# Performance work log

Hardware: AMD Instinct MI355X
Metric: run time of the kernel (lower is better)

## Reference

```python
import jax, jax.numpy as jnp
import numpy as np

B, SQ, SC, D = 16, 1024, 1024, 768
H = 2 * D  # 1536, fc width
NCLS = 2


def setup_inputs() -> dict:
    key = jax.random.key(0)
    ks = jax.random.split(key, 8)
    q = jax.random.normal(ks[0], (B, SQ, D), jnp.float32)
    c = jax.random.normal(ks[1], (B, SC, D), jnp.float32)
    mask_q = jax.random.randint(ks[2], (B, SQ), 0, 2).astype(jnp.int32)
    mask_c = jax.random.randint(ks[3], (B, SC), 0, 2).astype(jnp.int32)
    labels = jax.random.randint(ks[4], (B,), 0, NCLS)
    # torch nn.Linear convention: weight [out, in], y = x @ W.T + b
    W1 = jax.random.normal(ks[5], (H, H), jnp.float32) * 0.02
    b1 = jnp.zeros((H,), jnp.float32)
    W2 = jax.random.normal(ks[6], (NCLS, H), jnp.float32) * 0.02
    b2 = jnp.zeros((NCLS,), jnp.float32)
    return dict(q=q, c=c, mask_q=mask_q, mask_c=mask_c, labels=labels,
                W1=W1, b1=b1, W2=W2, b2=b2)


def reference(q, c, mask_q, mask_c, labels, W1, b1, W2, b2):
    # masked QK^T score matrix: [B, SQ, SC]
    s = jnp.einsum('bik,bjk->bij', q, c)
    s = s * mask_q[:, :, None].astype(s.dtype) * mask_c[:, None, :].astype(s.dtype)
    s = jnp.where(s == 0.0, -jnp.inf, s)  # x[x == 0.0] = -inf
    p = jnp.nan_to_num(jax.nn.softmax(s, axis=2))   # softmax over context axis
    pp = jnp.nan_to_num(jax.nn.softmax(s, axis=1))  # softmax over question axis
    a = jnp.einsum('bjk,bij->bk', c, p)   # weighted combine into context feats
    bb = jnp.einsum('bik,bij->bk', q, pp)  # weighted combine into question feats
    x = jnp.concatenate([a, bb], axis=1)  # [B, 1536]
    x = jnp.tanh(x @ W1.T + b1)           # fc1 + tanh (dropout = identity in eval)
    logits = x @ W2.T + b2                # fc2
    logp = jax.nn.log_softmax(logits, axis=1)  # LogSoftmax(dim=1)
    # NLLLoss (mean reduction)
    loss = -jnp.mean(jnp.take_along_axis(logp, labels[:, None], axis=1))
    return (loss, logp)
```

## Files before the change

### kernel.cpp

```cpp
#include <hip/hip_runtime.h>
#include <math.h>

#define B_   16
#define SQ_  1024
#define SC_  1024
#define D_   768
#define H_   1536
#define BK   32
#define LDK  40

typedef __attribute__((ext_vector_type(4))) float f32x4;
typedef __attribute__((ext_vector_type(8))) short bf16x8;

__device__ __forceinline__ unsigned cvtpk(float x, float y) {
  unsigned r;
  asm("v_cvt_pk_bf16_f32 %0, %1, %2" : "=v"(r) : "v"(x), "v"(y));
  return r;
}

__device__ __forceinline__ void split4(float4 v, uint2& hi, uint2& lo) {
  unsigned h01 = cvtpk(v.x, v.y);
  unsigned h23 = cvtpk(v.z, v.w);
  float h0 = __uint_as_float(h01 << 16);
  float h1 = __uint_as_float(h01 & 0xFFFF0000u);
  float h2 = __uint_as_float(h23 << 16);
  float h3 = __uint_as_float(h23 & 0xFFFF0000u);
  hi = make_uint2(h01, h23);
  lo = make_uint2(cvtpk(v.x - h0, v.y - h1), cvtpk(v.z - h2, v.w - h3));
}

__global__ __launch_bounds__(256) void compact_kernel(
    const int* __restrict__ mask_q, const int* __restrict__ mask_c,
    int* __restrict__ idx_q, int* __restrict__ idx_c, int* __restrict__ cnt)
{
  int which = blockIdx.x & 1;
  int b     = blockIdx.x >> 1;
  const int* m = (which ? mask_c : mask_q) + b * 1024;
  int* idx     = (which ? idx_c : idx_q) + b * 1024;

  __shared__ int tsum[256];
  int t = threadIdx.x;
  int v[4], s = 0;
#pragma unroll
  for (int e = 0; e < 4; ++e) { v[e] = (m[t * 4 + e] != 0) ? 1 : 0; s += v[e]; }
  tsum[t] = s;
  __syncthreads();
  for (int off = 1; off < 256; off <<= 1) {
    int add = (t >= off) ? tsum[t - off] : 0;
    __syncthreads();
    tsum[t] += add;
    __syncthreads();
  }
  int pos = tsum[t] - s;
#pragma unroll
  for (int e = 0; e < 4; ++e) {
    if (v[e]) idx[pos++] = t * 4 + e;
  }
  if (t == 255) cnt[b * 2 + which] = tsum[255];
}

__global__ __launch_bounds__(256) void gemm_mfma_kernel(
    const float* __restrict__ q, const float* __restrict__ c,
    const int* __restrict__ idx_q, const int* __restrict__ idx_c,
    const int* __restrict__ cnt, float* __restrict__ S)
{
  __shared__ unsigned short Ah[2][64][LDK];
  __shared__ unsigned short Al[2][64][LDK];
  __shared__ unsigned short Bh[2][64][LDK];
  __shared__ unsigned short Bl[2][64][LDK];

  const int b  = blockIdx.z;
  const int i0 = blockIdx.y * 64;
  const int j0 = blockIdx.x * 64;
  const int nq = cnt[2 * b], nc = cnt[2 * b + 1];
  if (i0 >= nq || j0 >= nc) return;

  const int t    = threadIdx.x;
  const int lane = t & 63;
  const int w    = t >> 6;

  const int srow = t >> 2;
  const int kc   = (t & 3) * 4;
  const int fr   = lane & 15;
  const int fq   = lane >> 4;
  const int kg   = fq * 8;

  const int rq = idx_q[b * 1024 + min(i0 + srow, nq - 1)];
  const int rc = idx_c[b * 1024 + min(j0 + srow, nc - 1)];
  const float* qrowP = q + ((size_t)b * SQ_ + rq) * D_;
  const float* crowP = c + ((size_t)b * SC_ + rc) * D_;

  f32x4 acc[4] = {};

  float4 av0 = *(const float4*)(qrowP + kc);
  float4 av1 = *(const float4*)(qrowP + kc + 16);
  float4 bv0 = *(const float4*)(crowP + kc);
  float4 bv1 = *(const float4*)(crowP + kc + 16);
  {
    uint2 hi, lo;
    split4(av0, hi, lo); *(uint2*)&Ah[0][srow][kc]      = hi; *(uint2*)&Al[0][srow][kc]      = lo;
    split4(av1, hi, lo); *(uint2*)&Ah[0][srow][kc + 16] = hi; *(uint2*)&Al[0][srow][kc + 16] = lo;
    split4(bv0, hi, lo); *(uint2*)&Bh[0][srow][kc]      = hi; *(uint2*)&Bl[0][srow][kc]      = lo;
    split4(bv1, hi, lo); *(uint2*)&Bh[0][srow][kc + 16] = hi; *(uint2*)&Bl[0][srow][kc + 16] = lo;
  }
  __syncthreads();

  int cur = 0;
  for (int k0 = 0; k0 < D_; k0 += BK) {
    const int next = k0 + BK;
    const bool has_next = (next < D_);
    if (has_next) {
      av0 = *(const float4*)(qrowP + next + kc);
      av1 = *(const float4*)(qrowP + next + kc + 16);
      bv0 = *(const float4*)(crowP + next + kc);
      bv1 = *(const float4*)(crowP + next + kc + 16);
    }

    bf16x8 b_h = *reinterpret_cast<const bf16x8*>(&Bh[cur][w * 16 + fr][kg]);
    bf16x8 b_l = *reinterpret_cast<const bf16x8*>(&Bl[cur][w * 16 + fr][kg]);
#pragma unroll
    for (int m = 0; m < 4; ++m) {
      bf16x8 a_h = *reinterpret_cast<const bf16x8*>(&Ah[cur][m * 16 + fr][kg]);
      bf16x8 a_l = *reinterpret_cast<const bf16x8*>(&Al[cur][m * 16 + fr][kg]);
      acc[m] = __builtin_amdgcn_mfma_f32_16x16x32_bf16(a_h, b_h, acc[m], 0, 0, 0);
      acc[m] = __builtin_amdgcn_mfma_f32_16x16x32_bf16(a_h, b_l, acc[m], 0, 0, 0);
      acc[m] = __builtin_amdgcn_mfma_f32_16x16x32_bf16(a_l, b_h, acc[m], 0, 0, 0);
    }

    if (has_next) {
      int nxt = cur ^ 1;
      uint2 hi, lo;
      split4(av0, hi, lo); *(uint2*)&Ah[nxt][srow][kc]      = hi; *(uint2*)&Al[nxt][srow][kc]      = lo;
      split4(av1, hi, lo); *(uint2*)&Ah[nxt][srow][kc + 16] = hi; *(uint2*)&Al[nxt][srow][kc + 16] = lo;
      split4(bv0, hi, lo); *(uint2*)&Bh[nxt][srow][kc]      = hi; *(uint2*)&Bl[nxt][srow][kc]      = lo;
      split4(bv1, hi, lo); *(uint2*)&Bh[nxt][srow][kc + 16] = hi; *(uint2*)&Bl[nxt][srow][kc + 16] = lo;
    }
    __syncthreads();
    cur ^= 1;
  }

  const int col = j0 + w * 16 + fr;
  const bool cok = (col < nc);
#pragma unroll
  for (int m = 0; m < 4; ++m) {
    int rbase = i0 + m * 16 + fq * 4;
    float* Sp = S + ((size_t)b * SQ_ + rbase) * SC_ + col;
#pragma unroll
    for (int rr = 0; rr < 4; ++rr) {
      float v = acc[m][rr];
      bool valid = ((rbase + rr) < nq) && cok && (v != 0.f);
      Sp[(size_t)rr * SC_] = valid ? v : -INFINITY;
    }
  }
}

__global__ __launch_bounds__(256) void row_stats_kernel(
    const float* __restrict__ S, const int* __restrict__ cnt,
    float* __restrict__ rmE, float* __restrict__ riE)
{
  int w    = threadIdx.x >> 6;
  int lane = threadIdx.x & 63;
  int row  = blockIdx.x * 4 + w;
  int b = row >> 10, i = row & 1023;
  int nq_pad = (cnt[2 * b] + 63) & ~63;
  if (i >= nq_pad) return;
  int nc_pad = (cnt[2 * b + 1] + 63) & ~63;
  const float4* Sr = (const float4*)(S + (size_t)row * SC_);

  float m = -INFINITY, s = 0.f;
  int n4 = nc_pad >> 2;
  for (int j4 = lane; j4 < n4; j4 += 64) {
    float4 v = Sr[j4];
    float vm = fmaxf(fmaxf(v.x, v.y), fmaxf(v.z, v.w));
    if (vm > m) { s *= __expf(m - vm); m = vm; }
    if (m > -INFINITY) {
      s += __expf(v.x - m) + __expf(v.y - m) + __expf(v.z - m) + __expf(v.w - m);
    }
  }
#pragma unroll
  for (int o = 32; o; o >>= 1) {
    float om = __shfl_xor(m, o);
    float os = __shfl_xor(s, o);
    float nm = fmaxf(m, om);
    float e1 = (m == nm) ? 1.f : __expf(m - nm);
    float e2 = (om == nm) ? 1.f : __expf(om - nm);
    s = s * e1 + os * e2;
    m = nm;
  }
  if (lane == 0) {
    bool dead = !(s > 0.f);
    rmE[row] = dead ? INFINITY : m;
    riE[row] = dead ? 0.f : 1.0f / s;
  }
}

__global__ __launch_bounds__(1024) void col_pass_kernel(
    const float* __restrict__ S, const int* __restrict__ cnt,
    const float* __restrict__ rmE, const float* __restrict__ riE,
    float* __restrict__ cmE, float* __restrict__ ciE,
    float* __restrict__ colsum_p)
{
  __shared__ float redm[1024], reds[1024], redp[1024];

  int b  = blockIdx.y;
  int j0 = blockIdx.x * 64;
  int nq_pad = (cnt[2 * b] + 63) & ~63;
  int nc_pad = (cnt[2 * b + 1] + 63) & ~63;
  if (j0 >= nc_pad) return;
  int t  = threadIdx.x;

  int j     = j0 + (t & 63);
  int wv    = t >> 6;
  int chunk = nq_pad >> 4;
  int i0    = wv * chunk;
  const float* Sb  = S + ((size_t)b * SQ_ + i0) * SC_ + j;
  const float* rmb = rmE + b * SQ_ + i0;
  const float* rib = riE + b * SQ_ + i0;

  float cm = -INFINITY, cs = 0.f, cp = 0.f;
  for (int ii = 0; ii < chunk; ++ii) {
    float v = Sb[(size_t)ii * SC_];
    cp += __expf(v - rmb[ii]) * rib[ii];
    if (v > cm) { cs = cs * __expf(cm - v) + 1.0f; cm = v; }
    else if (cm > -INFINITY) cs += __expf(v - cm);
  }

  redm[t] = cm; reds[t] = cs; redp[t] = cp;
  __syncthreads();
  if (t < 64) {
    float m = redm[t], s = reds[t], p = redp[t];
#pragma unroll
    for (int wv2 = 1; wv2 < 16; ++wv2) {
      float om = redm[wv2 * 64 + t], os = reds[wv2 * 64 + t];
      float nm = fmaxf(m, om);
      float e1 = (m == nm) ? 1.f : __expf(m - nm);
      float e2 = (om == nm) ? 1.f : __expf(om - nm);
      s = s * e1 + os * e2; m = nm;
      p += redp[wv2 * 64 + t];
    }
    bool dead = !(s > 0.f);
    cmE[b * SC_ + j0 + t] = dead ? INFINITY : m;
    ciE[b * SC_ + j0 + t] = dead ? 0.f : 1.0f / s;
    colsum_p[b * SC_ + j0 + t] = p;
  }
}

__global__ __launch_bounds__(256) void rowsum_pp_kernel(
    const float* __restrict__ S, const int* __restrict__ cnt,
    const float* __restrict__ cmE, const float* __restrict__ ciE,
    float* __restrict__ rowsum_pp)
{
  int t = threadIdx.x;
  int row0 = blockIdx.x * 4;
  int b = row0 >> 10;
  int nq = cnt[2 * b];
  if ((row0 & 1023) >= nq) return;
  int nc_pad = (cnt[2 * b + 1] + 63) & ~63;

  int w = t >> 6, lane = t & 63;
  int row = row0 + w;
  const float4* Sr  = (const float4*)(S + (size_t)row * SC_);
  const float4* cm4 = (const float4*)(cmE + b * SC_);
  const float4* ci4 = (const float4*)(ciE + b * SC_);

  float accv = 0.f;
  int n4 = nc_pad >> 2;
  for (int j4 = lane; j4 < n4; j4 += 64) {
    float4 v = Sr[j4];
    float4 cm = cm4[j4];
    float4 ci = ci4[j4];
    accv += __expf(v.x - cm.x) * ci.x;
    accv += __expf(v.y - cm.y) * ci.y;
    accv += __expf(v.z - cm.z) * ci.z;
    accv += __expf(v.w - cm.w) * ci.w;
  }
#pragma unroll
  for (int o = 32; o; o >>= 1) accv += __shfl_xor(accv, o);
  if (lane == 0) rowsum_pp[row] = accv;
}

__global__ __launch_bounds__(256) void combine_kernel(
    const float* __restrict__ q, const float* __restrict__ c,
    const int* __restrict__ idx_q, const int* __restrict__ idx_c,
    const int* __restrict__ cnt,
    const float* __restrict__ colsum_p, const float* __restrict__ rowsum_pp,
    float* __restrict__ Xp)
{
  int jc = blockIdx.x;
  int op = blockIdx.y;
  int b  = blockIdx.z;
  int t  = threadIdx.x;

  int n = op ? cnt[2 * b] : cnt[2 * b + 1];
  const float* src = op ? (q + (size_t)b * SQ_ * D_) : (c + (size_t)b * SC_ * D_);
  const float* wv  = op ? (rowsum_pp + b * SQ_) : (colsum_p + b * SC_);
  const int*   idx = (op ? idx_q : idx_c) + b * 1024;

  float a0 = 0.f, a1 = 0.f, a2 = 0.f;
  int je = min(jc * 32 + 32, n);
  for (int j = jc * 32; j < je; ++j) {
    float wj = wv[j];
    const float* r = src + (size_t)idx[j] * D_;
    a0 += wj * r[t];
    a1 += wj * r[t + 256];
    a2 += wj * r[t + 512];
  }
  float* xp = Xp + ((size_t)jc * B_ + b) * H_ + op * D_;
  xp[t] = a0; xp[t + 256] = a1; xp[t + 512] = a2;
}

__global__ __launch_bounds__(256) void reduce_x_kernel(
    const float* __restrict__ Xp, float* __restrict__ X)
{
  int idx = blockIdx.x * 256 + threadIdx.x;
  float s = 0.f;
#pragma unroll
  for (int ch = 0; ch < 32; ++ch) s += Xp[(size_t)ch * B_ * H_ + idx];
  X[idx] = s;
}

__global__ __launch_bounds__(256) void fc1_kernel(
    const float* __restrict__ X, const float* __restrict__ W1,
    const float* __restrict__ b1, float* __restrict__ Y)
{
  int w = threadIdx.x >> 6, lane = threadIdx.x & 63;
  int h = blockIdx.x * 4 + w;
  const float4* wr = (const float4*)(W1 + (size_t)h * H_);
  float4 wv[6];
#pragma unroll
  for (int it = 0; it < 6; ++it) wv[it] = wr[it * 64 + lane];
  float bias = b1[h];

  for (int b = 0; b < B_; ++b) {
    const float4* x = (const float4*)(X + (size_t)b * H_);
    float accv = 0.f;
#pragma unroll
    for (int it = 0; it < 6; ++it) {
      float4 xv = x[it * 64 + lane];
      accv += xv.x * wv[it].x + xv.y * wv[it].y + xv.z * wv[it].z + xv.w * wv[it].w;
    }
#pragma unroll
    for (int o = 32; o; o >>= 1) accv += __shfl_xor(accv, o);
    if (lane == 0) Y[(size_t)b * H_ + h] = tanhf(accv + bias);
  }
}

__global__ __launch_bounds__(64) void fc2_loss_kernel(
    const float* __restrict__ Y, const float* __restrict__ W2,
    const float* __restrict__ b2, const int* __restrict__ labels,
    float* __restrict__ out)
{
  __shared__ float logp_s[B_][2];
  int t = threadIdx.x;
  if (t < 2 * B_) {
    int b = t >> 1, n = t & 1;
    const float* y = Y + (size_t)b * H_;
    const float* w = W2 + (size_t)n * H_;
    float accv = b2[n];
    for (int k = 0; k < H_; ++k) accv += y[k] * w[k];
    logp_s[b][n] = accv;
  }
  __syncthreads();
  if (t < B_) {
    float l0 = logp_s[t][0], l1 = logp_s[t][1];
    float m = fmaxf(l0, l1);
    float lse = m + logf(expf(l0 - m) + expf(l1 - m));
    logp_s[t][0] = l0 - lse;
    logp_s[t][1] = l1 - lse;
  }
  __syncthreads();
  if (t < 2 * B_) out[1 + t] = logp_s[t >> 1][t & 1];
  if (t == 0) {
    float loss = 0.f;
    for (int b = 0; b < B_; ++b) loss -= logp_s[b][labels[b]];
    out[0] = loss / (float)B_;
  }
}

extern "C" void kernel_launch(void* const* d_in, const int* in_sizes, int n_in,
                              void* d_out, int out_size, void* d_ws, size_t ws_size,
                              hipStream_t stream) {
  const float* q      = (const float*)d_in[0];
  const float* c      = (const float*)d_in[1];
  const int*   mask_q = (const int*)d_in[2];
  const int*   mask_c = (const int*)d_in[3];
  const int*   labels = (const int*)d_in[4];
  const float* W1     = (const float*)d_in[5];
  const float* b1     = (const float*)d_in[6];
  const float* W2     = (const float*)d_in[7];
  const float* b2     = (const float*)d_in[8];
  float* out = (float*)d_out;

  float* ws        = (float*)d_ws;
  float* S         = ws;
  float* rmE       = ws + (size_t)B_ * SQ_ * SC_;
  float* riE       = rmE + B_ * SQ_;
  float* cmE       = riE + B_ * SQ_;
  float* ciE       = cmE + B_ * SC_;
  float* colsum_p  = ciE + B_ * SC_;
  float* rowsum_pp = colsum_p + B_ * SC_;
  int*   cnt       = (int*)(rowsum_pp + B_ * SQ_);
  int*   idx_q     = cnt + 2 * B_;
  int*   idx_c     = idx_q + B_ * SQ_;
  float* Xp        = ws;
  float* X         = ws + 32 * B_ * H_;
  float* Y         = X + B_ * H_;

  compact_kernel<<<2 * B_, 256, 0, stream>>>(mask_q, mask_c, idx_q, idx_c, cnt);

  dim3 g1(SC_ / 64, SQ_ / 64, B_);
  gemm_mfma_kernel<<<g1, 256, 0, stream>>>(q, c, idx_q, idx_c, cnt, S);

  row_stats_kernel<<<(B_ * SQ_) / 4, 256, 0, stream>>>(S, cnt, rmE, riE);
  col_pass_kernel<<<dim3(SC_ / 64, B_), 1024, 0, stream>>>(S, cnt, rmE, riE,
                                                           cmE, ciE, colsum_p);
  rowsum_pp_kernel<<<(B_ * SQ_) / 4, 256, 0, stream>>>(S, cnt, cmE, ciE, rowsum_pp);

  combine_kernel<<<dim3(32, 2, B_), 256, 0, stream>>>(q, c, idx_q, idx_c, cnt,
                                                      colsum_p, rowsum_pp, Xp);
  reduce_x_kernel<<<(B_ * H_) / 256, 256, 0, stream>>>(Xp, X);
  fc1_kernel<<<H_ / 4, 256, 0, stream>>>(X, W1, b1, Y);
  fc2_loss_kernel<<<1, 64, 0, stream>>>(Y, W2, b2, labels, out);
}
```

Before: 158.4 us.

## Fuse softmax denominators into GEMM epilogue with persistent tile scheduler

The GEMM epilogue now computes unshifted exponentials in double precision, using a custom exp that avoids overflow, and atomically accumulates the row and column softmax denominators. This removes the separate row-stats pass and the max-tracking column pass. A persistent atomic tile queue over only the valid compacted tiles replaces the sparse 3D grid. A single pass2 kernel then produces both weighted sums, and the combine kernel writes X with atomics instead of a partial buffer plus a reduce kernel. The trade-offs are heavy double-precision atomics, per-row float atomics in pass2, and reliance on the scores staying within double exponent range.

```diff
diff --git a/kernel.cpp b/kernel.cpp
--- a/kernel.cpp
+++ b/kernel.cpp
@@ -29,6 +29,15 @@
   lo = make_uint2(cvtpk(v.x - h0, v.y - h1), cvtpk(v.z - h2, v.w - h3));
 }
 
+__device__ __forceinline__ double exp_pos(float s) {
+  float t = s * 1.4426950408889634f;
+  float n = floorf(t);
+  float p = exp2f(t - n);
+  long long e = (long long)n;
+  double scale = __longlong_as_double((unsigned long long)(e + 1023LL) << 52);
+  return (double)p * scale;
+}
+
 __global__ __launch_bounds__(256) void compact_kernel(
     const int* __restrict__ mask_q, const int* __restrict__ mask_c,
     int* __restrict__ idx_q, int* __restrict__ idx_c, int* __restrict__ cnt)
@@ -59,232 +68,207 @@
   if (t == 255) cnt[b * 2 + which] = tsum[255];
 }
 
+__global__ void tile_setup_kernel(const int* __restrict__ cnt, int* __restrict__ tmeta)
+{
+  if (threadIdx.x == 0) {
+    int off = 0;
+    for (int b = 0; b < B_; ++b) {
+      int ntq = (cnt[2 * b] + 63) >> 6;
+      int ntc = (cnt[2 * b + 1] + 63) >> 6;
+      tmeta[1 + b]  = off;
+      tmeta[17 + b] = ntc;
+      off += ntq * ntc;
+    }
+    tmeta[0]  = off;
+    tmeta[33] = 0;
+  }
+}
+
 __global__ __launch_bounds__(256) void gemm_mfma_kernel(
     const float* __restrict__ q, const float* __restrict__ c,
     const int* __restrict__ idx_q, const int* __restrict__ idx_c,
-    const int* __restrict__ cnt, float* __restrict__ S)
+    const int* __restrict__ cnt, int* __restrict__ tmeta,
+    float* __restrict__ S, double* __restrict__ R, double* __restrict__ C)
 {
   __shared__ unsigned short Ah[2][64][LDK];
   __shared__ unsigned short Al[2][64][LDK];
   __shared__ unsigned short Bh[2][64][LDK];
   __shared__ unsigned short Bl[2][64][LDK];
-
-  const int b  = blockIdx.z;
-  const int i0 = blockIdx.y * 64;
-  const int j0 = blockIdx.x * 64;
-  const int nq = cnt[2 * b], nc = cnt[2 * b + 1];
-  if (i0 >= nq || j0 >= nc) return;
+  __shared__ int tidx_s;
 
   const int t    = threadIdx.x;
   const int lane = t & 63;
   const int w    = t >> 6;
-
   const int srow = t >> 2;
   const int kc   = (t & 3) * 4;
   const int fr   = lane & 15;
   const int fq   = lane >> 4;
   const int kg   = fq * 8;
 
-  const int rq = idx_q[b * 1024 + min(i0 + srow, nq - 1)];
-  const int rc = idx_c[b * 1024 + min(j0 + srow, nc - 1)];
-  const float* qrowP = q + ((size_t)b * SQ_ + rq) * D_;
-  const float* crowP = c + ((size_t)b * SC_ + rc) * D_;
-
-  f32x4 acc[4] = {};
-
-  float4 av0 = *(const float4*)(qrowP + kc);
-  float4 av1 = *(const float4*)(qrowP + kc + 16);
-  float4 bv0 = *(const float4*)(crowP + kc);
-  float4 bv1 = *(const float4*)(crowP + kc + 16);
-  {
-    uint2 hi, lo;
-    split4(av0, hi, lo); *(uint2*)&Ah[0][srow][kc]      = hi; *(uint2*)&Al[0][srow][kc]      = lo;
-    split4(av1, hi, lo); *(uint2*)&Ah[0][srow][kc + 16] = hi; *(uint2*)&Al[0][srow][kc + 16] = lo;
-    split4(bv0, hi, lo); *(uint2*)&Bh[0][srow][kc]      = hi; *(uint2*)&Bl[0][srow][kc]      = lo;
-    split4(bv1, hi, lo); *(uint2*)&Bh[0][srow][kc + 16] = hi; *(uint2*)&Bl[0][srow][kc + 16] = lo;
-  }
-  __syncthreads();
-
-  int cur = 0;
-  for (int k0 = 0; k0 < D_; k0 += BK) {
-    const int next = k0 + BK;
-    const bool has_next = (next < D_);
-    if (has_next) {
-      av0 = *(const float4*)(qrowP + next + kc);
-      av1 = *(const float4*)(qrowP + next + kc + 16);
-      bv0 = *(const float4*)(crowP + next + kc);
-      bv1 = *(const float4*)(crowP + next + kc + 16);
-    }
-
-    bf16x8 b_h = *reinterpret_cast<const bf16x8*>(&Bh[cur][w * 16 + fr][kg]);
-    bf16x8 b_l = *reinterpret_cast<const bf16x8*>(&Bl[cur][w * 16 + fr][kg]);
+  const int total = tmeta[0];
+
+  while (true) {
+    if (t == 0) tidx_s = atomicAdd(&tmeta[33], 1);
+    __syncthreads();
+    const int idx = tidx_s;
+    if (idx >= total) break;
+
+    int bb = 0;
+#pragma unroll
+    for (int k = 1; k < 16; ++k) bb += (idx >= tmeta[1 + k]) ? 1 : 0;
+    const int rem = idx - tmeta[1 + bb];
+    const int ntc = tmeta[17 + bb];
+    const int ty  = rem / ntc;
+    const int tx  = rem - ty * ntc;
+    const int i0  = ty * 64, j0 = tx * 64;
+    const int nq  = cnt[2 * bb], nc = cnt[2 * bb + 1];
+
+    const int rq = idx_q[bb * 1024 + min(i0 + srow, nq - 1)];
+    const int rc = idx_c[bb * 1024 + min(j0 + srow, nc - 1)];
+    const float* qrowP = q + ((size_t)bb * SQ_ + rq) * D_;
+    const float* crowP = c + ((size_t)bb * SC_ + rc) * D_;
+
+    f32x4 acc[4] = {};
+
+    float4 av0 = *(const float4*)(qrowP + kc);
+    float4 av1 = *(const float4*)(qrowP + kc + 16);
+    float4 bv0 = *(const float4*)(crowP + kc);
+    float4 bv1 = *(const float4*)(crowP + kc + 16);
+    {
+      uint2 hi, lo;
+      split4(av0, hi, lo); *(uint2*)&Ah[0][srow][kc]      = hi; *(uint2*)&Al[0][srow][kc]      = lo;
+      split4(av1, hi, lo); *(uint2*)&Ah[0][srow][kc + 16] = hi; *(uint2*)&Al[0][srow][kc + 16] = lo;
+      split4(bv0, hi, lo); *(uint2*)&Bh[0][srow][kc]      = hi; *(uint2*)&Bl[0][srow][kc]      = lo;
+      split4(bv1, hi, lo); *(uint2*)&Bh[0][srow][kc + 16] = hi; *(uint2*)&Bl[0][srow][kc + 16] = lo;
+    }
+    __syncthreads();
+
+    int cur = 0;
+    for (int k0 = 0; k0 < D_; k0 += BK) {
+      const int next = k0 + BK;
+      const bool has_next = (next < D_);
+      if (has_next) {
+        av0 = *(const float4*)(qrowP + next + kc);
+        av1 = *(const float4*)(qrowP + next + kc + 16);
+        bv0 = *(const float4*)(crowP + next + kc);
+        bv1 = *(const float4*)(crowP + next + kc + 16);
+      }
+
+      bf16x8 b_h = *reinterpret_cast<const bf16x8*>(&Bh[cur][w * 16 + fr][kg]);
+      bf16x8 b_l = *reinterpret_cast<const bf16x8*>(&Bl[cur][w * 16 + fr][kg]);
+#pragma unroll
+      for (int m = 0; m < 4; ++m) {
+        bf16x8 a_h = *reinterpret_cast<const bf16x8*>(&Ah[cur][m * 16 + fr][kg]);
+        bf16x8 a_l = *reinterpret_cast<const bf16x8*>(&Al[cur][m * 16 + fr][kg]);
+        acc[m] = __builtin_amdgcn_mfma_f32_16x16x32_bf16(a_h, b_h, acc[m], 0, 0, 0);
+        acc[m] = __builtin_amdgcn_mfma_f32_16x16x32_bf16(a_h, b_l, acc[m], 0, 0, 0);
+        acc[m] = __builtin_amdgcn_mfma_f32_16x16x32_bf16(a_l, b_h, acc[m], 0, 0, 0);
+      }
+
+      if (has_next) {
+        int nxt = cur ^ 1;
+        uint2 hi, lo;
+        split4(av0, hi, lo); *(uint2*)&Ah[nxt][srow][kc]      = hi; *(uint2*)&Al[nxt][srow][kc]      = lo;
+        split4(av1, hi, lo); *(uint2*)&Ah[nxt][srow][kc + 16] = hi; *(uint2*)&Al[nxt][srow][kc + 16] = lo;
+        split4(bv0, hi, lo); *(uint2*)&Bh[nxt][srow][kc]      = hi; *(uint2*)&Bl[nxt][srow][kc]      = lo;
+        split4(bv1, hi, lo); *(uint2*)&Bh[nxt][srow][kc + 16] = hi; *(uint2*)&Bl[nxt][srow][kc + 16] = lo;
+      }
+      __syncthreads();
+      cur ^= 1;
+    }
+
+    double* rowAcc = reinterpret_cast<double*>(&Ah[0][0][0]);
+    const int col = j0 + w * 16 + fr;
+    const bool cok = (col < nc);
+    double colSum = 0.0;
 #pragma unroll
     for (int m = 0; m < 4; ++m) {
-      bf16x8 a_h = *reinterpret_cast<const bf16x8*>(&Ah[cur][m * 16 + fr][kg]);
-      bf16x8 a_l = *reinterpret_cast<const bf16x8*>(&Al[cur][m * 16 + fr][kg]);
-      acc[m] = __builtin_amdgcn_mfma_f32_16x16x32_bf16(a_h, b_h, acc[m], 0, 0, 0);
-      acc[m] = __builtin_amdgcn_mfma_f32_16x16x32_bf16(a_h, b_l, acc[m], 0, 0, 0);
-      acc[m] = __builtin_amdgcn_mfma_f32_16x16x32_bf16(a_l, b_h, acc[m], 0, 0, 0);
-    }
-
-    if (has_next) {
-      int nxt = cur ^ 1;
-      uint2 hi, lo;
-      split4(av0, hi, lo); *(uint2*)&Ah[nxt][srow][kc]      = hi; *(uint2*)&Al[nxt][srow][kc]      = lo;
-      split4(av1, hi, lo); *(uint2*)&Ah[nxt][srow][kc + 16] = hi; *(uint2*)&Al[nxt][srow][kc + 16] = lo;
-      split4(bv0, hi, lo); *(uint2*)&Bh[nxt][srow][kc]      = hi; *(uint2*)&Bl[nxt][srow][kc]      = lo;
-      split4(bv1, hi, lo); *(uint2*)&Bh[nxt][srow][kc + 16] = hi; *(uint2*)&Bl[nxt][srow][kc + 16] = lo;
-    }
-    __syncthreads();
-    cur ^= 1;
-  }
-
-  const int col = j0 + w * 16 + fr;
-  const bool cok = (col < nc);
-#pragma unroll
-  for (int m = 0; m < 4; ++m) {
-    int rbase = i0 + m * 16 + fq * 4;
-    float* Sp = S + ((size_t)b * SQ_ + rbase) * SC_ + col;
-#pragma unroll
-    for (int rr = 0; rr < 4; ++rr) {
-      float v = acc[m][rr];
-      bool valid = ((rbase + rr) < nq) && cok && (v != 0.f);
-      Sp[(size_t)rr * SC_] = valid ? v : -INFINITY;
-    }
-  }
-}
-
-__global__ __launch_bounds__(256) void row_stats_kernel(
+      int rbase = i0 + m * 16 + fq * 4;
+      float* Sp = S + ((size_t)bb * SQ_ + rbase) * SC_ + col;
+#pragma unroll
+      for (int rr = 0; rr < 4; ++rr) {
+        float v = acc[m][rr];
+        bool valid = ((rbase + rr) < nq) && cok && (v != 0.f);
+        Sp[(size_t)rr * SC_] = valid ? v : -INFINITY;
+        double e = valid ? exp_pos(v) : 0.0;
+        colSum += e;
+        double rsum = e;
+        rsum += __shfl_xor(rsum, 1);
+        rsum += __shfl_xor(rsum, 2);
+        rsum += __shfl_xor(rsum, 4);
+        rsum += __shfl_xor(rsum, 8);
+        if (fr == 0) rowAcc[w * 64 + m * 16 + fq * 4 + rr] = rsum;
+      }
+    }
+    colSum += __shfl_xor(colSum, 16);
+    colSum += __shfl_xor(colSum, 32);
+    if (fq == 0 && cok) atomicAdd(&C[bb * SC_ + col], colSum);
+    __syncthreads();
+    if (t < 64) {
+      double rs = rowAcc[t] + rowAcc[64 + t] + rowAcc[128 + t] + rowAcc[192 + t];
+      if ((i0 + t) < nq && rs != 0.0) atomicAdd(&R[bb * SQ_ + i0 + t], rs);
+    }
+    __syncthreads();
+  }
+}
+
+__global__ __launch_bounds__(1024) void pass2_kernel(
     const float* __restrict__ S, const int* __restrict__ cnt,
-    float* __restrict__ rmE, float* __restrict__ riE)
-{
-  int w    = threadIdx.x >> 6;
-  int lane = threadIdx.x & 63;
-  int row  = blockIdx.x * 4 + w;
-  int b = row >> 10, i = row & 1023;
-  int nq_pad = (cnt[2 * b] + 63) & ~63;
-  if (i >= nq_pad) return;
-  int nc_pad = (cnt[2 * b + 1] + 63) & ~63;
-  const float4* Sr = (const float4*)(S + (size_t)row * SC_);
-
-  float m = -INFINITY, s = 0.f;
-  int n4 = nc_pad >> 2;
-  for (int j4 = lane; j4 < n4; j4 += 64) {
-    float4 v = Sr[j4];
-    float vm = fmaxf(fmaxf(v.x, v.y), fmaxf(v.z, v.w));
-    if (vm > m) { s *= __expf(m - vm); m = vm; }
-    if (m > -INFINITY) {
-      s += __expf(v.x - m) + __expf(v.y - m) + __expf(v.z - m) + __expf(v.w - m);
-    }
-  }
-#pragma unroll
-  for (int o = 32; o; o >>= 1) {
-    float om = __shfl_xor(m, o);
-    float os = __shfl_xor(s, o);
-    float nm = fmaxf(m, om);
-    float e1 = (m == nm) ? 1.f : __expf(m - nm);
-    float e2 = (om == nm) ? 1.f : __expf(om - nm);
-    s = s * e1 + os * e2;
-    m = nm;
-  }
-  if (lane == 0) {
-    bool dead = !(s > 0.f);
-    rmE[row] = dead ? INFINITY : m;
-    riE[row] = dead ? 0.f : 1.0f / s;
-  }
-}
-
-__global__ __launch_bounds__(1024) void col_pass_kernel(
-    const float* __restrict__ S, const int* __restrict__ cnt,
-    const float* __restrict__ rmE, const float* __restrict__ riE,
-    float* __restrict__ cmE, float* __restrict__ ciE,
-    float* __restrict__ colsum_p)
-{
-  __shared__ float redm[1024], reds[1024], redp[1024];
+    const double* __restrict__ R, const double* __restrict__ C,
+    float* __restrict__ cp, float* __restrict__ rpp)
+{
+  __shared__ float lnR_lds[SQ_];
+  __shared__ float red[16][64];
 
   int b  = blockIdx.y;
   int j0 = blockIdx.x * 64;
   int nq_pad = (cnt[2 * b] + 63) & ~63;
   int nc_pad = (cnt[2 * b + 1] + 63) & ~63;
   if (j0 >= nc_pad) return;
-  int t  = threadIdx.x;
-
-  int j     = j0 + (t & 63);
-  int wv    = t >> 6;
+  int t = threadIdx.x;
+
+  if (t < nq_pad) {
+    double Ri = R[b * SQ_ + t];
+    lnR_lds[t] = (Ri > 0.0) ? (float)log(Ri) : INFINITY;
+  }
+  __syncthreads();
+
+  int lane = t & 63, wv = t >> 6;
+  int j = j0 + lane;
+  double Cj = C[b * SC_ + j];
+  float lnCj = (Cj > 0.0) ? (float)log(Cj) : INFINITY;
+
   int chunk = nq_pad >> 4;
-  int i0    = wv * chunk;
-  const float* Sb  = S + ((size_t)b * SQ_ + i0) * SC_ + j;
-  const float* rmb = rmE + b * SQ_ + i0;
-  const float* rib = riE + b * SQ_ + i0;
-
-  float cm = -INFINITY, cs = 0.f, cp = 0.f;
+  int i0 = wv * chunk;
+  const float* Sb = S + ((size_t)b * SQ_ + i0) * SC_ + j;
+
+  float cpAcc = 0.f;
   for (int ii = 0; ii < chunk; ++ii) {
+    int i = i0 + ii;
     float v = Sb[(size_t)ii * SC_];
-    cp += __expf(v - rmb[ii]) * rib[ii];
-    if (v > cm) { cs = cs * __expf(cm - v) + 1.0f; cm = v; }
-    else if (cm > -INFINITY) cs += __expf(v - cm);
-  }
-
-  redm[t] = cm; reds[t] = cs; redp[t] = cp;
+    cpAcc += __expf(v - lnR_lds[i]);
+    float e2 = __expf(v - lnCj);
+#pragma unroll
+    for (int o = 32; o; o >>= 1) e2 += __shfl_xor(e2, o);
+    if (lane == 0) atomicAdd(&rpp[b * SQ_ + i], e2);
+  }
+
+  red[wv][lane] = cpAcc;
   __syncthreads();
   if (t < 64) {
-    float m = redm[t], s = reds[t], p = redp[t];
-#pragma unroll
-    for (int wv2 = 1; wv2 < 16; ++wv2) {
-      float om = redm[wv2 * 64 + t], os = reds[wv2 * 64 + t];
-      float nm = fmaxf(m, om);
-      float e1 = (m == nm) ? 1.f : __expf(m - nm);
-      float e2 = (om == nm) ? 1.f : __expf(om - nm);
-      s = s * e1 + os * e2; m = nm;
-      p += redp[wv2 * 64 + t];
-    }
-    bool dead = !(s > 0.f);
-    cmE[b * SC_ + j0 + t] = dead ? INFINITY : m;
-    ciE[b * SC_ + j0 + t] = dead ? 0.f : 1.0f / s;
-    colsum_p[b * SC_ + j0 + t] = p;
-  }
-}
-
-__global__ __launch_bounds__(256) void rowsum_pp_kernel(
-    const float* __restrict__ S, const int* __restrict__ cnt,
-    const float* __restrict__ cmE, const float* __restrict__ ciE,
-    float* __restrict__ rowsum_pp)
-{
-  int t = threadIdx.x;
-  int row0 = blockIdx.x * 4;
-  int b = row0 >> 10;
-  int nq = cnt[2 * b];
-  if ((row0 & 1023) >= nq) return;
-  int nc_pad = (cnt[2 * b + 1] + 63) & ~63;
-
-  int w = t >> 6, lane = t & 63;
-  int row = row0 + w;
-  const float4* Sr  = (const float4*)(S + (size_t)row * SC_);
-  const float4* cm4 = (const float4*)(cmE + b * SC_);
-  const float4* ci4 = (const float4*)(ciE + b * SC_);
-
-  float accv = 0.f;
-  int n4 = nc_pad >> 2;
-  for (int j4 = lane; j4 < n4; j4 += 64) {
-    float4 v = Sr[j4];
-    float4 cm = cm4[j4];
-    float4 ci = ci4[j4];
-    accv += __expf(v.x - cm.x) * ci.x;
-    accv += __expf(v.y - cm.y) * ci.y;
-    accv += __expf(v.z - cm.z) * ci.z;
-    accv += __expf(v.w - cm.w) * ci.w;
-  }
-#pragma unroll
-  for (int o = 32; o; o >>= 1) accv += __shfl_xor(accv, o);
-  if (lane == 0) rowsum_pp[row] = accv;
+    float s = 0.f;
+#pragma unroll
+    for (int k = 0; k < 16; ++k) s += red[k][t];
+    cp[b * SC_ + j0 + t] = s;
+  }
 }
 
 __global__ __launch_bounds__(256) void combine_kernel(
     const float* __restrict__ q, const float* __restrict__ c,
     const int* __restrict__ idx_q, const int* __restrict__ idx_c,
     const int* __restrict__ cnt,
-    const float* __restrict__ colsum_p, const float* __restrict__ rowsum_pp,
-    float* __restrict__ Xp)
+    const float* __restrict__ cp, const float* __restrict__ rpp,
+    float* __restrict__ X)
 {
   int jc = blockIdx.x;
   int op = blockIdx.y;
@@ -293,7 +277,7 @@
 
   int n = op ? cnt[2 * b] : cnt[2 * b + 1];
   const float* src = op ? (q + (size_t)b * SQ_ * D_) : (c + (size_t)b * SC_ * D_);
-  const float* wv  = op ? (rowsum_pp + b * SQ_) : (colsum_p + b * SC_);
+  const float* wv  = op ? (rpp + b * SQ_) : (cp + b * SC_);
   const int*   idx = (op ? idx_q : idx_c) + b * 1024;
 
   float a0 = 0.f, a1 = 0.f, a2 = 0.f;
@@ -305,18 +289,10 @@
     a1 += wj * r[t + 256];
     a2 += wj * r[t + 512];
   }
-  float* xp = Xp + ((size_t)jc * B_ + b) * H_ + op * D_;
-  xp[t] = a0; xp[t + 256] = a1; xp[t + 512] = a2;
-}
-
-__global__ __launch_bounds__(256) void reduce_x_kernel(
-    const float* __restrict__ Xp, float* __restrict__ X)
-{
-  int idx = blockIdx.x * 256 + threadIdx.x;
-  float s = 0.f;
-#pragma unroll
-  for (int ch = 0; ch < 32; ++ch) s += Xp[(size_t)ch * B_ * H_ + idx];
-  X[idx] = s;
+  float* xp = X + (size_t)b * H_ + op * D_;
+  atomicAdd(&xp[t], a0);
+  atomicAdd(&xp[t + 256], a1);
+  atomicAdd(&xp[t + 512], a2);
 }
 
 __global__ __launch_bounds__(256) void fc1_kernel(
@@ -391,34 +367,32 @@
   const float* b2     = (const float*)d_in[8];
   float* out = (float*)d_out;
 
-  float* ws        = (float*)d_ws;
-  float* S         = ws;
-  float* rmE       = ws + (size_t)B_ * SQ_ * SC_;
-  float* riE       = rmE + B_ * SQ_;
-  float* cmE       = riE + B_ * SQ_;
-  float* ciE       = cmE + B_ * SC_;
-  float* colsum_p  = ciE + B_ * SC_;
-  float* rowsum_pp = colsum_p + B_ * SC_;
-  int*   cnt       = (int*)(rowsum_pp + B_ * SQ_);
-  int*   idx_q     = cnt + 2 * B_;
-  int*   idx_c     = idx_q + B_ * SQ_;
-  float* Xp        = ws;
-  float* X         = ws + 32 * B_ * H_;
-  float* Y         = X + B_ * H_;
+  float*  ws   = (float*)d_ws;
+  float*  S    = ws;
+  double* R    = (double*)(ws + (size_t)B_ * SQ_ * SC_);
+  double* C    = R + B_ * SQ_;
+  float*  cp   = (float*)(C + B_ * SC_);
+  float*  rpp  = cp + B_ * SC_;
+  int*    cnt  = (int*)(rpp + B_ * SQ_);
+  int*    tmeta = cnt + 2 * B_;
+  int*    idx_q = tmeta + 34;
+  int*    idx_c = idx_q + B_ * SQ_;
+  float*  X    = ws;
+  float*  Y    = ws + B_ * H_;
+
+  (void)hipMemsetAsync((void*)R, 0, (size_t)(2 * B_ * SQ_) * sizeof(double)
+                              + (size_t)(2 * B_ * SC_) * sizeof(float), stream);
 
   compact_kernel<<<2 * B_, 256, 0, stream>>>(mask_q, mask_c, idx_q, idx_c, cnt);
-
-  dim3 g1(SC_ / 64, SQ_ / 64, B_);
-  gemm_mfma_kernel<<<g1, 256, 0, stream>>>(q, c, idx_q, idx_c, cnt, S);
-
-  row_stats_kernel<<<(B_ * SQ_) / 4, 256, 0, stream>>>(S, cnt, rmE, riE);
-  col_pass_kernel<<<dim3(SC_ / 64, B_), 1024, 0, stream>>>(S, cnt, rmE, riE,
-                                                           cmE, ciE, colsum_p);
-  rowsum_pp_kernel<<<(B_ * SQ_) / 4, 256, 0, stream>>>(S, cnt, cmE, ciE, rowsum_pp);
-
+  tile_setup_kernel<<<1, 64, 0, stream>>>(cnt, tmeta);
+
+  gemm_mfma_kernel<<<1024, 256, 0, stream>>>(q, c, idx_q, idx_c, cnt, tmeta, S, R, C);
+
+  pass2_kernel<<<dim3(SC_ / 64, B_), 1024, 0, stream>>>(S, cnt, R, C, cp, rpp);
+
+  (void)hipMemsetAsync((void*)X, 0, (size_t)B_ * H_ * sizeof(float), stream);
   combine_kernel<<<dim3(32, 2, B_), 256, 0, stream>>>(q, c, idx_q, idx_c, cnt,
-                                                      colsum_p, rowsum_pp, Xp);
-  reduce_x_kernel<<<(B_ * H_) / 256, 256, 0, stream>>>(Xp, X);
+                                                      cp, rpp, X);
   fc1_kernel<<<H_ / 4, 256, 0, stream>>>(X, W1, b1, Y);
   fc2_loss_kernel<<<1, 64, 0, stream>>>(Y, W2, b2, labels, out);
 }
```

Result: slower. 164.0 us (+3.5%).

## Swizzle merged hi/lo GEMM LDS tiles and fold X reduction into atomics

Applied to the files above, without the earlier changes.

The GEMM now keeps the hi and lo bf16 halves of each row in a single 64-wide LDS row with an XOR swizzle, instead of four padded arrays. This is meant to cut LDS bank conflicts and the padding overhead on the MFMA operand reads. Separately, combine_kernel now atomically adds its partial sums straight into X, which compact_kernel zeroes first, so the Xp partial buffer and the reduce_x kernel launch are gone. The trade is atomic contention on X and a summation order that is no longer deterministic.

```diff
diff --git a/kernel.cpp b/kernel.cpp
--- a/kernel.cpp
+++ b/kernel.cpp
@@ -6,8 +6,6 @@
 #define SC_  1024
 #define D_   768
 #define H_   1536
-#define BK   32
-#define LDK  40
 
 typedef __attribute__((ext_vector_type(4))) float f32x4;
 typedef __attribute__((ext_vector_type(8))) short bf16x8;
@@ -31,15 +29,19 @@
 
 __global__ __launch_bounds__(256) void compact_kernel(
     const int* __restrict__ mask_q, const int* __restrict__ mask_c,
-    int* __restrict__ idx_q, int* __restrict__ idx_c, int* __restrict__ cnt)
+    int* __restrict__ idx_q, int* __restrict__ idx_c, int* __restrict__ cnt,
+    float* __restrict__ zeroB, int lenB)
 {
   int which = blockIdx.x & 1;
   int b     = blockIdx.x >> 1;
   const int* m = (which ? mask_c : mask_q) + b * 1024;
   int* idx     = (which ? idx_c : idx_q) + b * 1024;
 
+  int t = threadIdx.x;
+  int gid = blockIdx.x * 256 + t;
+  for (int i = gid; i < lenB; i += 32 * 256) zeroB[i] = 0.f;
+
   __shared__ int tsum[256];
-  int t = threadIdx.x;
   int v[4], s = 0;
 #pragma unroll
   for (int e = 0; e < 4; ++e) { v[e] = (m[t * 4 + e] != 0) ? 1 : 0; s += v[e]; }
@@ -64,76 +66,96 @@
     const int* __restrict__ idx_q, const int* __restrict__ idx_c,
     const int* __restrict__ cnt, float* __restrict__ S)
 {
-  __shared__ unsigned short Ah[2][64][LDK];
-  __shared__ unsigned short Al[2][64][LDK];
-  __shared__ unsigned short Bh[2][64][LDK];
-  __shared__ unsigned short Bl[2][64][LDK];
-
-  const int b  = blockIdx.z;
+  __shared__ unsigned short Ahl[2][64 * 64];
+  __shared__ unsigned short Bhl[2][64 * 64];
+
+  const int bb = blockIdx.z;
   const int i0 = blockIdx.y * 64;
   const int j0 = blockIdx.x * 64;
-  const int nq = cnt[2 * b], nc = cnt[2 * b + 1];
+  const int nq = cnt[2 * bb], nc = cnt[2 * bb + 1];
   if (i0 >= nq || j0 >= nc) return;
 
   const int t    = threadIdx.x;
   const int lane = t & 63;
   const int w    = t >> 6;
-
   const int srow = t >> 2;
-  const int kc   = (t & 3) * 4;
+  const int sc8  = (t & 3) * 8;
+  const int swzS = (srow & 7) << 3;
   const int fr   = lane & 15;
   const int fq   = lane >> 4;
-  const int kg   = fq * 8;
-
-  const int rq = idx_q[b * 1024 + min(i0 + srow, nq - 1)];
-  const int rc = idx_c[b * 1024 + min(j0 + srow, nc - 1)];
-  const float* qrowP = q + ((size_t)b * SQ_ + rq) * D_;
-  const float* crowP = c + ((size_t)b * SC_ + rc) * D_;
+
+  const int rq = idx_q[bb * 1024 + min(i0 + srow, nq - 1)];
+  const int rc = idx_c[bb * 1024 + min(j0 + srow, nc - 1)];
+  const float* qrowP = q + ((size_t)bb * SQ_ + rq) * D_ + sc8;
+  const float* crowP = c + ((size_t)bb * SC_ + rc) * D_ + sc8;
 
   f32x4 acc[4] = {};
 
-  float4 av0 = *(const float4*)(qrowP + kc);
-  float4 av1 = *(const float4*)(qrowP + kc + 16);
-  float4 bv0 = *(const float4*)(crowP + kc);
-  float4 bv1 = *(const float4*)(crowP + kc + 16);
+  float4 a0 = *(const float4*)(qrowP);
+  float4 a1 = *(const float4*)(qrowP + 4);
+  float4 b0 = *(const float4*)(crowP);
+  float4 b1 = *(const float4*)(crowP + 4);
   {
     uint2 hi, lo;
-    split4(av0, hi, lo); *(uint2*)&Ah[0][srow][kc]      = hi; *(uint2*)&Al[0][srow][kc]      = lo;
-    split4(av1, hi, lo); *(uint2*)&Ah[0][srow][kc + 16] = hi; *(uint2*)&Al[0][srow][kc + 16] = lo;
-    split4(bv0, hi, lo); *(uint2*)&Bh[0][srow][kc]      = hi; *(uint2*)&Bl[0][srow][kc]      = lo;
-    split4(bv1, hi, lo); *(uint2*)&Bh[0][srow][kc + 16] = hi; *(uint2*)&Bl[0][srow][kc + 16] = lo;
+    split4(a0, hi, lo);
+    *(uint2*)&Ahl[0][srow * 64 + ((sc8 + 0) ^ swzS)]      = hi;
+    *(uint2*)&Ahl[0][srow * 64 + ((32 + sc8 + 0) ^ swzS)] = lo;
+    split4(a1, hi, lo);
+    *(uint2*)&Ahl[0][srow * 64 + ((sc8 + 4) ^ swzS)]      = hi;
+    *(uint2*)&Ahl[0][srow * 64 + ((32 + sc8 + 4) ^ swzS)] = lo;
+    split4(b0, hi, lo);
+    *(uint2*)&Bhl[0][srow * 64 + ((sc8 + 0) ^ swzS)]      = hi;
+    *(uint2*)&Bhl[0][srow * 64 + ((32 + sc8 + 0) ^ swzS)] = lo;
+    split4(b1, hi, lo);
+    *(uint2*)&Bhl[0][srow * 64 + ((sc8 + 4) ^ swzS)]      = hi;
+    *(uint2*)&Bhl[0][srow * 64 + ((32 + sc8 + 4) ^ swzS)] = lo;
   }
   __syncthreads();
 
   int cur = 0;
-  for (int k0 = 0; k0 < D_; k0 += BK) {
-    const int next = k0 + BK;
+  for (int k0 = 0; k0 < D_; k0 += 32) {
+    const int next = k0 + 32;
     const bool has_next = (next < D_);
     if (has_next) {
-      av0 = *(const float4*)(qrowP + next + kc);
-      av1 = *(const float4*)(qrowP + next + kc + 16);
-      bv0 = *(const float4*)(crowP + next + kc);
-      bv1 = *(const float4*)(crowP + next + kc + 16);
-    }
-
-    bf16x8 b_h = *reinterpret_cast<const bf16x8*>(&Bh[cur][w * 16 + fr][kg]);
-    bf16x8 b_l = *reinterpret_cast<const bf16x8*>(&Bl[cur][w * 16 + fr][kg]);
+      a0 = *(const float4*)(qrowP + next);
+      a1 = *(const float4*)(qrowP + next + 4);
+      b0 = *(const float4*)(crowP + next);
+      b1 = *(const float4*)(crowP + next + 4);
+    }
+
+    bf16x8 b_h, b_l;
+    {
+      const int row = w * 16 + fr;
+      const int sw  = (row & 7) << 3;
+      b_h = *(const bf16x8*)&Bhl[cur][row * 64 + ((fq * 8) ^ sw)];
+      b_l = *(const bf16x8*)&Bhl[cur][row * 64 + ((32 + fq * 8) ^ sw)];
+    }
 #pragma unroll
     for (int m = 0; m < 4; ++m) {
-      bf16x8 a_h = *reinterpret_cast<const bf16x8*>(&Ah[cur][m * 16 + fr][kg]);
-      bf16x8 a_l = *reinterpret_cast<const bf16x8*>(&Al[cur][m * 16 + fr][kg]);
+      const int row = m * 16 + fr;
+      const int sw  = (row & 7) << 3;
+      bf16x8 a_h = *(const bf16x8*)&Ahl[cur][row * 64 + ((fq * 8) ^ sw)];
+      bf16x8 a_l = *(const bf16x8*)&Ahl[cur][row * 64 + ((32 + fq * 8) ^ sw)];
       acc[m] = __builtin_amdgcn_mfma_f32_16x16x32_bf16(a_h, b_h, acc[m], 0, 0, 0);
       acc[m] = __builtin_amdgcn_mfma_f32_16x16x32_bf16(a_h, b_l, acc[m], 0, 0, 0);
       acc[m] = __builtin_amdgcn_mfma_f32_16x16x32_bf16(a_l, b_h, acc[m], 0, 0, 0);
     }
 
     if (has_next) {
-      int nxt = cur ^ 1;
+      const int nxt = cur ^ 1;
       uint2 hi, lo;
-      split4(av0, hi, lo); *(uint2*)&Ah[nxt][srow][kc]      = hi; *(uint2*)&Al[nxt][srow][kc]      = lo;
-      split4(av1, hi, lo); *(uint2*)&Ah[nxt][srow][kc + 16] = hi; *(uint2*)&Al[nxt][srow][kc + 16] = lo;
-      split4(bv0, hi, lo); *(uint2*)&Bh[nxt][srow][kc]      = hi; *(uint2*)&Bl[nxt][srow][kc]      = lo;
-      split4(bv1, hi, lo); *(uint2*)&Bh[nxt][srow][kc + 16] = hi; *(uint2*)&Bl[nxt][srow][kc + 16] = lo;
+      split4(a0, hi, lo);
+      *(uint2*)&Ahl[nxt][srow * 64 + ((sc8 + 0) ^ swzS)]      = hi;
+      *(uint2*)&Ahl[nxt][srow * 64 + ((32 + sc8 + 0) ^ swzS)] = lo;
+      split4(a1, hi, lo);
+      *(uint2*)&Ahl[nxt][srow * 64 + ((sc8 + 4) ^ swzS)]      = hi;
+      *(uint2*)&Ahl[nxt][srow * 64 + ((32 + sc8 + 4) ^ swzS)] = lo;
+      split4(b0, hi, lo);
+      *(uint2*)&Bhl[nxt][srow * 64 + ((sc8 + 0) ^ swzS)]      = hi;
+      *(uint2*)&Bhl[nxt][srow * 64 + ((32 + sc8 + 0) ^ swzS)] = lo;
+      split4(b1, hi, lo);
+      *(uint2*)&Bhl[nxt][srow * 64 + ((sc8 + 4) ^ swzS)]      = hi;
+      *(uint2*)&Bhl[nxt][srow * 64 + ((32 + sc8 + 4) ^ swzS)] = lo;
     }
     __syncthreads();
     cur ^= 1;
@@ -144,7 +166,7 @@
 #pragma unroll
   for (int m = 0; m < 4; ++m) {
     int rbase = i0 + m * 16 + fq * 4;
-    float* Sp = S + ((size_t)b * SQ_ + rbase) * SC_ + col;
+    float* Sp = S + ((size_t)bb * SQ_ + rbase) * SC_ + col;
 #pragma unroll
     for (int rr = 0; rr < 4; ++rr) {
       float v = acc[m][rr];
@@ -283,8 +305,8 @@
     const float* __restrict__ q, const float* __restrict__ c,
     const int* __restrict__ idx_q, const int* __restrict__ idx_c,
     const int* __restrict__ cnt,
-    const float* __restrict__ colsum_p, const float* __restrict__ rowsum_pp,
-    float* __restrict__ Xp)
+    const float* __restrict__ cp, const float* __restrict__ rpp,
+    float* __restrict__ X)
 {
   int jc = blockIdx.x;
   int op = blockIdx.y;
@@ -293,7 +315,7 @@
 
   int n = op ? cnt[2 * b] : cnt[2 * b + 1];
   const float* src = op ? (q + (size_t)b * SQ_ * D_) : (c + (size_t)b * SC_ * D_);
-  const float* wv  = op ? (rowsum_pp + b * SQ_) : (colsum_p + b * SC_);
+  const float* wv  = op ? (rpp + b * SQ_) : (cp + b * SC_);
   const int*   idx = (op ? idx_q : idx_c) + b * 1024;
 
   float a0 = 0.f, a1 = 0.f, a2 = 0.f;
@@ -305,18 +327,10 @@
     a1 += wj * r[t + 256];
     a2 += wj * r[t + 512];
   }
-  float* xp = Xp + ((size_t)jc * B_ + b) * H_ + op * D_;
-  xp[t] = a0; xp[t + 256] = a1; xp[t + 512] = a2;
-}
-
-__global__ __launch_bounds__(256) void reduce_x_kernel(
-    const float* __restrict__ Xp, float* __restrict__ X)
-{
-  int idx = blockIdx.x * 256 + threadIdx.x;
-  float s = 0.f;
-#pragma unroll
-  for (int ch = 0; ch < 32; ++ch) s += Xp[(size_t)ch * B_ * H_ + idx];
-  X[idx] = s;
+  float* xp = X + (size_t)b * H_ + op * D_;
+  atomicAdd(&xp[t], a0);
+  atomicAdd(&xp[t + 256], a1);
+  atomicAdd(&xp[t + 512], a2);
 }
 
 __global__ __launch_bounds__(256) void fc1_kernel(
@@ -391,34 +405,34 @@
   const float* b2     = (const float*)d_in[8];
   float* out = (float*)d_out;
 
-  float* ws        = (float*)d_ws;
-  float* S         = ws;
-  float* rmE       = ws + (size_t)B_ * SQ_ * SC_;
-  float* riE       = rmE + B_ * SQ_;
-  float* cmE       = riE + B_ * SQ_;
-  float* ciE       = cmE + B_ * SC_;
-  float* colsum_p  = ciE + B_ * SC_;
-  float* rowsum_pp = colsum_p + B_ * SC_;
-  int*   cnt       = (int*)(rowsum_pp + B_ * SQ_);
-  int*   idx_q     = cnt + 2 * B_;
-  int*   idx_c     = idx_q + B_ * SQ_;
-  float* Xp        = ws;
-  float* X         = ws + 32 * B_ * H_;
-  float* Y         = X + B_ * H_;
-
-  compact_kernel<<<2 * B_, 256, 0, stream>>>(mask_q, mask_c, idx_q, idx_c, cnt);
+  float*  ws    = (float*)d_ws;
+  float*  S     = ws;
+  float*  rmE   = ws + (size_t)B_ * SQ_ * SC_;
+  float*  riE   = rmE + B_ * SQ_;
+  float*  cmE   = riE + B_ * SQ_;
+  float*  ciE   = cmE + B_ * SC_;
+  float*  cp    = ciE + B_ * SC_;
+  float*  rpp   = cp + B_ * SC_;
+  int*    cnt   = (int*)(rpp + B_ * SQ_);
+  int*    idx_q = cnt + 2 * B_;
+  int*    idx_c = idx_q + B_ * SQ_;
+  float*  X     = (float*)(idx_c + B_ * SC_);
+  float*  Y     = X + B_ * H_;
+  const int lenB = B_ * H_;
+
+  compact_kernel<<<2 * B_, 256, 0, stream>>>(mask_q, mask_c, idx_q, idx_c, cnt,
+                                             X, lenB);
 
   dim3 g1(SC_ / 64, SQ_ / 64, B_);
   gemm_mfma_kernel<<<g1, 256, 0, stream>>>(q, c, idx_q, idx_c, cnt, S);
 
   row_stats_kernel<<<(B_ * SQ_) / 4, 256, 0, stream>>>(S, cnt, rmE, riE);
   col_pass_kernel<<<dim3(SC_ / 64, B_), 1024, 0, stream>>>(S, cnt, rmE, riE,
-                                                           cmE, ciE, colsum_p);
-  rowsum_pp_kernel<<<(B_ * SQ_) / 4, 256, 0, stream>>>(S, cnt, cmE, ciE, rowsum_pp);
+                                                           cmE, ciE, cp);
+  rowsum_pp_kernel<<<(B_ * SQ_) / 4, 256, 0, stream>>>(S, cnt, cmE, ciE, rpp);
 
   combine_kernel<<<dim3(32, 2, B_), 256, 0, stream>>>(q, c, idx_q, idx_c, cnt,
-                                                      colsum_p, rowsum_pp, Xp);
-  reduce_x_kernel<<<(B_ * H_) / 256, 256, 0, stream>>>(Xp, X);
+                                                      cp, rpp, X);
   fc1_kernel<<<H_ / 4, 256, 0, stream>>>(X, W1, b1, Y);
   fc2_loss_kernel<<<1, 64, 0, stream>>>(Y, W2, b2, labels, out);
 }
```

New measurement: 167.4 us. +5.7%, slower.
